# Performance work log

Hardware: AMD Instinct MI355X
Metric: run time of the kernel (lower is better)

Reference implementation:

```python
import jax, jax.numpy as jnp
import numpy as np
from jax import lax

HEADS = 8
DIM_HEAD = 64
SCALE = DIM_HEAD ** -0.5

def conv2d(x, w, stride=1, pad=0):
    return lax.conv_general_dilated(
        x, w, window_strides=(stride, stride),
        padding=[(pad, pad), (pad, pad)],
        dimension_numbers=("NCHW", "OIHW", "NCHW"))

def setup_inputs() -> dict:
    key = jax.random.key(0)
    ks = jax.random.split(key, 5)
    b, dim, H, W = 8, 256, 32, 32
    inner = HEADS * DIM_HEAD  # 512
    x = jax.random.normal(ks[0], (b, dim, H, W), jnp.float32)
    Wq = jax.random.normal(ks[1], (inner, dim, 1, 1), jnp.float32) * 0.05
    Wkv = jax.random.normal(ks[2], (2 * inner, dim, 3, 3), jnp.float32) * 0.05
    Wout = jax.random.normal(ks[3], (dim, inner, 1, 1), jnp.float32) * 0.05
    bout = jnp.zeros((dim,), jnp.float32)
    return {"x": x, "Wq": Wq, "Wkv": Wkv, "Wout": Wout, "bout": bout}

def reference(x, Wq, Wkv, Wout, bout):
    b = x.shape[0]
    h, d = HEADS, DIM_HEAD
    q = conv2d(x, Wq, stride=1, pad=0)        # [b, h*d, H, W]
    kv = conv2d(x, Wkv, stride=1, pad=1)      # [b, 2*h*d, H, W]
    k, v = jnp.split(kv, 2, axis=1)
    out_h, out_w = q.shape[-2:]

    def to_bhnd(t):
        # b (h d) x y -> b h (x y) d
        B, _, X, Y = t.shape
        return t.reshape(B, h, d, X * Y).transpose(0, 1, 3, 2)

    q, k, v = map(to_bhnd, (q, k, v))
    dots = jnp.einsum("bhid,bhjd->bhij", q, k) * SCALE
    attn = jax.nn.softmax(dots, axis=-1)
    out = jnp.einsum("bhij,bhjd->bhid", attn, v)  # [b, h, n, d]
    # b h (x y) d -> b (h d) x y
    out = out.transpose(0, 1, 3, 2).reshape(b, h * d, out_h, out_w)
    out = jax.nn.gelu(out, approximate=False)
    out = conv2d(out, Wout, stride=1, pad=0) + bout[None, :, None, None]
    return out
```

## Files before the change

### kernel.cpp

```cpp
#include <hip/hip_runtime.h>
#include <math.h>

#define BATCH 8
#define DIM   256
#define NPIX  1024
#define DHEAD 64
#define INNER 512
#define KVCH  1024
#define PPIX  1156

typedef _Float16 half8 __attribute__((ext_vector_type(8)));
typedef _Float16 half4 __attribute__((ext_vector_type(4)));
typedef float    f32x4 __attribute__((ext_vector_type(4)));
typedef float    f32x16 __attribute__((ext_vector_type(16)));
#define MFMA16(a, b, c) __builtin_amdgcn_mfma_f32_16x16x32_f16(a, b, c, 0, 0, 0)
#define MFMA32(a, b, c) __builtin_amdgcn_mfma_f32_32x32x16_f16(a, b, c, 0, 0, 0)

static __device__ __forceinline__ float gelu_f(float v) {
    return 0.5f * v * (1.0f + erff(v * 0.70710678118654752440f));
}

static __device__ __forceinline__ void gload16(const _Float16* g, _Float16* l) {
    __builtin_amdgcn_global_load_lds(
        (const __attribute__((address_space(1))) unsigned int*)g,
        (__attribute__((address_space(3))) unsigned int*)l, 16, 0, 0);
}

__global__ __launch_bounds__(256) void prep_kernel(
    const float* __restrict__ Wq, const float* __restrict__ Wkv,
    const float* __restrict__ Wout, const float* __restrict__ x,
    _Float16* __restrict__ Aq, _Float16* __restrict__ Akv,
    _Float16* __restrict__ Aout, _Float16* __restrict__ xtp)
{
    const int bid = blockIdx.x, tid = threadIdx.x;
    if (bid < 512) {
        __shared__ float ts[64][65];
        const int pt = (bid & 15) * 64, ic0 = ((bid >> 4) & 3) * 64, b = bid >> 6;
        const float* xb = x + (((size_t)(b * DIM + ic0)) << 10) + pt;
#pragma unroll
        for (int e = tid; e < 4096; e += 256) {
            int i = e >> 6, p = e & 63;
            ts[i][p] = xb[((size_t)i << 10) + p];
        }
        __syncthreads();
#pragma unroll
        for (int e = tid; e < 512; e += 256) {
            int p = e >> 3, ig = e & 7;
            int gp = pt + p, y = gp >> 5, xc = gp & 31;
            half8 v;
#pragma unroll
            for (int u = 0; u < 8; ++u) v[u] = (_Float16)ts[ig * 8 + u][p];
            *(half8*)&xtp[((size_t)b * PPIX + (y + 1) * 34 + xc + 1) * 256 + ic0 + ig * 8] = v;
        }
    } else if (bid < 10752) {
        const int e = (bid - 512) * 256 + tid;
        if (e < 131072) Aq[e] = (_Float16)Wq[e];
        const int e2 = e - 131072;
        if (e2 >= 0 && e2 < 2359296) {
            int oc = e2 / 2304, r = e2 - oc * 2304;
            int s = r >> 8, ic = r & 255;
            Akv[e2] = (_Float16)Wkv[oc * 2304 + ic * 9 + s];
        }
        const int e3 = e - 131072 - 2359296;
        if (e3 >= 0 && e3 < 131072) Aout[e3] = (_Float16)Wout[e3];
    } else {
        const int he = (bid - 10752) * 256 + tid;
        if (he < 270336) {
            int b = he / 33792;
            int r = he - b * 33792;
            int hp = r >> 8, ic = r & 255;
            int row, col;
            if (hp < 34)      { row = 0;  col = hp; }
            else if (hp < 68) { row = 33; col = hp - 34; }
            else { int k2 = hp - 68; row = 1 + (k2 >> 1); col = (k2 & 1) * 33; }
            xtp[((size_t)b * PPIX + row * 34 + col) * 256 + ic] = (_Float16)0.f;
        }
    }
}

__global__ __launch_bounds__(256) void qkv_gemm_kernel(
    const _Float16* __restrict__ Akv, const _Float16* __restrict__ Aq,
    const _Float16* __restrict__ xtp, _Float16* __restrict__ qt,
    _Float16* __restrict__ ktp, _Float16* __restrict__ vb)
{
    __shared__ _Float16 As0[128 * 64];
    __shared__ _Float16 As1[128 * 64];
    __shared__ _Float16 Bs0[128 * 64];
    __shared__ _Float16 Bs1[128 * 64];
    const int nt = blockIdx.x, mt = blockIdx.y, b = blockIdx.z;
    const bool QBLK = (mt >= 8);
    const int tid = threadIdx.x;
    const int w = tid >> 6, lane = tid & 63;
    const int l31 = lane & 31, kh = lane >> 5;
    const int m0 = (QBLK ? mt - 8 : mt) * 128, p0 = nt * 128;
    const int wm = (w >> 1) * 64, wn = (w & 1) * 64;

    const int srow = lane >> 3;
    const int scol = ((lane & 7) ^ srow) * 8;

    const _Float16* abase = QBLK ? Aq : Akv;
    const int astride = QBLK ? 256 : 2304;
    const int ktend = QBLK ? 4 : 36;

    const _Float16* agp[4];
    const _Float16* bgp[4];
#pragma unroll
    for (int c = 0; c < 4; ++c) {
        int row = (w * 4 + c) * 8 + srow;
        agp[c] = abase + (size_t)(m0 + row) * astride + scol;
        int p = p0 + row, py = p >> 5, px = p & 31;
        bgp[c] = xtp + ((size_t)b * PPIX + (py + 1) * 34 + px + 1) * 256 + scol;
    }

    f32x16 acc[2][2];
#pragma unroll
    for (int mf = 0; mf < 2; ++mf)
#pragma unroll
        for (int nf = 0; nf < 2; ++nf)
#pragma unroll
            for (int r = 0; r < 16; ++r) acc[mf][nf][r] = 0.f;

    auto STAGE = [&](int kt, _Float16* Asb, _Float16* Bsb) {
        const int s = QBLK ? 4 : (kt >> 2);
        const int doff = (s / 3 - 1) * 34 + (s - (s / 3) * 3) - 1;
        const int boff = doff * 256 + (kt & 3) * 64;
#pragma unroll
        for (int c = 0; c < 4; ++c)
            gload16(agp[c] + kt * 64, &Asb[(w * 4 + c) * 512]);
#pragma unroll
        for (int c = 0; c < 4; ++c)
            gload16(bgp[c] + boff, &Bsb[(w * 4 + c) * 512]);
    };

    auto COMPUTE = [&](const _Float16* Asb, const _Float16* Bsb) {
#pragma unroll
        for (int kc = 0; kc < 4; ++kc) {
            const int cx = ((((kc << 1) | kh) ^ (l31 & 7)) << 3);
            half8 af[2], bf[2];
#pragma unroll
            for (int mf = 0; mf < 2; ++mf)
                af[mf] = *(const half8*)&Asb[(wm + mf * 32 + l31) * 64 + cx];
#pragma unroll
            for (int nf = 0; nf < 2; ++nf)
                bf[nf] = *(const half8*)&Bsb[(wn + nf * 32 + l31) * 64 + cx];
#pragma unroll
            for (int mf = 0; mf < 2; ++mf)
#pragma unroll
                for (int nf = 0; nf < 2; ++nf)
                    acc[mf][nf] = MFMA32(af[mf], bf[nf], acc[mf][nf]);
        }
    };

    STAGE(0, As0, Bs0);
    __syncthreads();

    for (int kt2 = 0; kt2 < ktend; kt2 += 2) {
        STAGE(kt2 + 1, As1, Bs1);
        COMPUTE(As0, Bs0);
        __syncthreads();
        if (kt2 + 2 < ktend) STAGE(kt2 + 2, As0, Bs0);
        COMPUTE(As1, Bs1);
        __syncthreads();
    }

#pragma unroll
    for (int mf = 0; mf < 2; ++mf) {
        const int mbase = m0 + wm + mf * 32;
        if (!QBLK && mbase >= 512) {
#pragma unroll
            for (int nf = 0; nf < 2; ++nf) {
                const int pix = p0 + wn + nf * 32 + l31;
#pragma unroll
                for (int reg = 0; reg < 16; ++reg) {
                    const int mv = mbase - 512 + (reg & 3) + 8 * (reg >> 2) + 4 * kh;
                    vb[(((size_t)(b * 512 + mv)) << 10) + pix] =
                        (_Float16)acc[mf][nf][reg];
                }
            }
        } else {
            const int h = mbase >> 6;
            const int dbase = (mbase & 63) + kh * 4;
            _Float16* dst = QBLK ? qt : ktp;
#pragma unroll
            for (int nf = 0; nf < 2; ++nf) {
                const int pix = p0 + wn + nf * 32 + l31;
#pragma unroll
                for (int g = 0; g < 4; ++g) {
                    half4 v4;
#pragma unroll
                    for (int r = 0; r < 4; ++r) {
                        float vv = acc[mf][nf][g * 4 + r];
                        if (QBLK) vv *= 0.125f;
                        v4[r] = (_Float16)vv;
                    }
                    *(half4*)&dst[((((size_t)(b * 8 + h)) << 10) + pix) * 64 + dbase + g * 8] = v4;
                }
            }
        }
    }
}

template<int M, int K, int KROW>
__global__ __launch_bounds__(256) void out_gemm_kernel(
    const _Float16* __restrict__ A, const _Float16* __restrict__ act,
    float* __restrict__ Cout, const float* __restrict__ bias)
{
    __shared__ _Float16 As[128 * 64];
    __shared__ _Float16 Bs[64 * 64];
    const int nt = blockIdx.x, mt = blockIdx.y, b = blockIdx.z;
    const int tid = threadIdx.x;
    const int w = tid >> 6, lane = tid & 63;
    const int quad = lane >> 4, l15 = lane & 15;
    const int m0 = mt * 128, p0 = nt * 64;
    const int wm = w * 32;
    const f32x4 Z4 = {0.f, 0.f, 0.f, 0.f};

    const int srow = lane >> 3;
    const int scol = ((lane & 7) ^ srow) * 8;

    const _Float16* agp[4];
#pragma unroll
    for (int c = 0; c < 4; ++c) {
        int row = (w * 4 + c) * 8 + srow;
        agp[c] = A + (size_t)(m0 + row) * K + scol;
    }
    const _Float16* bgp[2];
#pragma unroll
    for (int c = 0; c < 2; ++c) {
        int row = (w * 2 + c) * 8 + srow;
        bgp[c] = act + (size_t)(b * NPIX + p0 + row) * KROW + scol;
    }

    f32x4 acc[2][4];
#pragma unroll
    for (int mi = 0; mi < 2; ++mi)
#pragma unroll
        for (int ni = 0; ni < 4; ++ni) acc[mi][ni] = Z4;

    for (int kt = 0; kt < K / 64; ++kt) {
        __syncthreads();
#pragma unroll
        for (int c = 0; c < 4; ++c)
            gload16(agp[c] + kt * 64, &As[(w * 4 + c) * 512]);
#pragma unroll
        for (int c = 0; c < 2; ++c)
            gload16(bgp[c] + kt * 64, &Bs[(w * 2 + c) * 512]);
        __syncthreads();
#pragma unroll
        for (int ks = 0; ks < 2; ++ks) {
            half8 av[2], bv[4];
#pragma unroll
            for (int mi = 0; mi < 2; ++mi) {
                const int r = wm + mi * 16 + l15;
                av[mi] = *(const half8*)&As[r * 64 + (((ks * 4 + quad) ^ (l15 & 7)) << 3)];
            }
#pragma unroll
            for (int ni = 0; ni < 4; ++ni) {
                const int r = ni * 16 + l15;
                bv[ni] = *(const half8*)&Bs[r * 64 + (((ks * 4 + quad) ^ (l15 & 7)) << 3)];
            }
#pragma unroll
            for (int mi = 0; mi < 2; ++mi)
#pragma unroll
                for (int ni = 0; ni < 4; ++ni)
                    acc[mi][ni] = MFMA16(av[mi], bv[ni], acc[mi][ni]);
        }
    }

#pragma unroll
    for (int mi = 0; mi < 2; ++mi) {
#pragma unroll
        for (int r = 0; r < 4; ++r) {
            const int m = m0 + wm + mi * 16 + quad * 4 + r;
            const float bv = bias[m];
#pragma unroll
            for (int ni = 0; ni < 4; ++ni) {
                const int pix = p0 + ni * 16 + l15;
                Cout[(((size_t)(b * M + m)) << 10) + pix] = acc[mi][ni][r] + bv;
            }
        }
    }
}

__global__ __launch_bounds__(256) void attn_kernel(
    const _Float16* __restrict__ qt,
    const _Float16* __restrict__ ktp,
    const _Float16* __restrict__ vbb,
    _Float16* __restrict__ gout)
{
    __shared__ _Float16 Ks[128 * 64];
    __shared__ _Float16 Vs[64 * 128];
    __shared__ _Float16 Pb[128 * 128];
    const int qtile = blockIdx.x, bh = blockIdx.y;
    const int b = bh >> 3, h = bh & 7;
    const int p0 = qtile * 128;
    const int tid = threadIdx.x;
    const int w = tid >> 6, lane = tid & 63;
    const int quad = lane >> 4, l15 = lane & 15;
    const f32x4 Z4 = {0.f, 0.f, 0.f, 0.f};

    half8 ones;
#pragma unroll
    for (int u = 0; u < 8; ++u) ones[u] = (_Float16)1.0f;

    half8 qf[2][2];
    {
        const _Float16* qrow =
            qt + ((((size_t)(bh)) << 10) + p0 + w * 32 + l15) * 64;
#pragma unroll
        for (int iff = 0; iff < 2; ++iff)
#pragma unroll
            for (int ks = 0; ks < 2; ++ks)
                qf[iff][ks] = *(const half8*)(qrow + iff * 16 * 64 + ks * 32 + quad * 8);
    }

    const _Float16* kbase = ktp + ((size_t)bh << 16);
    const _Float16* vbase = vbb + (((size_t)(b * 512 + h * 64)) << 10);

    f32x4 oacc[4][2];
#pragma unroll
    for (int mf = 0; mf < 4; ++mf)
#pragma unroll
        for (int iff = 0; iff < 2; ++iff) oacc[mf][iff] = Z4;
    f32x4 racc[2] = {Z4, Z4};

    const int kchunk = (lane & 7) ^ (lane >> 3);
    for (int kt = 0; kt < 8; ++kt) {
        const int pk = kt * 128;
        __syncthreads();
        const _Float16* kg = kbase + (size_t)pk * 64;
#pragma unroll
        for (int i = 0; i < 4; ++i) {
            const int t = i * 4 + w;
            gload16(kg + (t * 8 + (lane >> 3)) * 64 + kchunk * 8, &Ks[t * 512]);
        }
#pragma unroll
        for (int i = 0; i < 4; ++i) {
            const int t = i * 4 + w;
            const int vd = t * 4 + (lane >> 4);
            gload16(vbase + ((size_t)vd << 10) + pk + (((lane & 15) ^ (vd & 15)) << 3),
                    &Vs[t * 512]);
        }
        __syncthreads();

#pragma unroll
        for (int g = 0; g < 2; ++g) {
            f32x4 s[4][2];
#pragma unroll
            for (int jf2 = 0; jf2 < 4; ++jf2) {
                const int jr = (g * 4 + jf2) * 16 + l15;
                const half8 ka0 = *(const half8*)&Ks[jr * 64 + ((quad ^ (l15 & 7)) << 3)];
                const half8 ka1 = *(const half8*)&Ks[jr * 64 + (((4 + quad) ^ (l15 & 7)) << 3)];
#pragma unroll
                for (int iff = 0; iff < 2; ++iff) {
                    s[jf2][iff] = MFMA16(ka0, qf[iff][0], Z4);
                    s[jf2][iff] = MFMA16(ka1, qf[iff][1], s[jf2][iff]);
                }
            }
#pragma unroll
            for (int jf2 = 0; jf2 < 4; ++jf2) {
#pragma unroll
                for (int iff = 0; iff < 2; ++iff) {
                    half4 pv4;
#pragma unroll
                    for (int r = 0; r < 4; ++r)
                        pv4[r] = (_Float16)__expf(s[jf2][iff][r] - 8.0f);
                    const int i = w * 32 + iff * 16 + l15;
                    const int c = ((g * 4 + jf2) << 1) + (quad >> 1);
                    *(half4*)&Pb[i * 128 + ((c ^ l15) << 3) + ((quad & 1) << 2)] = pv4;
                }
            }
        }
#pragma unroll
        for (int kc = 0; kc < 4; ++kc) {
            half8 bv[2];
#pragma unroll
            for (int iff = 0; iff < 2; ++iff) {
                const int i = w * 32 + iff * 16 + l15;
                bv[iff] = *(const half8*)&Pb[i * 128 + (((kc * 4 + quad) ^ l15) << 3)];
                racc[iff] = MFMA16(ones, bv[iff], racc[iff]);
            }
#pragma unroll
            for (int mf = 0; mf < 4; ++mf) {
                const int vr = mf * 16 + l15;
                const half8 va = *(const half8*)&Vs[vr * 128 + (((kc * 4 + quad) ^ l15) << 3)];
#pragma unroll
                for (int iff = 0; iff < 2; ++iff)
                    oacc[mf][iff] = MFMA16(va, bv[iff], oacc[mf][iff]);
            }
        }
    }

    float rinv[2];
#pragma unroll
    for (int iff = 0; iff < 2; ++iff) rinv[iff] = 1.f / racc[iff][0];

    __syncthreads();
    _Float16* scr = Pb;
#pragma unroll
    for (int mf = 0; mf < 4; ++mf) {
#pragma unroll
        for (int iff = 0; iff < 2; ++iff) {
            half4 o4;
#pragma unroll
            for (int r = 0; r < 4; ++r)
                o4[r] = (_Float16)gelu_f(oacc[mf][iff][r] * rinv[iff]);
            const int i = w * 32 + iff * 16 + l15;
            *(half4*)&scr[i * 72 + mf * 16 + quad * 4] = o4;
        }
    }
    __syncthreads();
    _Float16* go = gout + ((size_t)(b * NPIX + p0)) * INNER + h * 64;
#pragma unroll
    for (int it = 0; it < 4; ++it) {
        const int e = tid + it * 256;
        const int p = e >> 3, dg = e & 7;
        *(half8*)(go + (size_t)p * INNER + dg * 8) = *(const half8*)&scr[p * 72 + dg * 8];
    }
}

extern "C" void kernel_launch(void* const* d_in, const int* in_sizes, int n_in,
                              void* d_out, int out_size, void* d_ws, size_t ws_size,
                              hipStream_t stream)
{
    const float* x    = (const float*)d_in[0];
    const float* Wq   = (const float*)d_in[1];
    const float* Wkv  = (const float*)d_in[2];
    const float* Wout = (const float*)d_in[3];
    const float* bout = (const float*)d_in[4];
    float* out = (float*)d_out;

    _Float16* xtp  = (_Float16*)d_ws;
    _Float16* Aq   = xtp  + (size_t)BATCH * PPIX * DIM;
    _Float16* Akv  = Aq   + (size_t)INNER * DIM;
    _Float16* Aout = Akv  + (size_t)KVCH * 2304;
    _Float16* qt   = Aout + (size_t)DIM * INNER;
    _Float16* vb   = qt   + (size_t)BATCH * NPIX * INNER;
    _Float16* ktp  = vb   + (size_t)BATCH * NPIX * INNER;
    _Float16* gout = ktp  + (size_t)BATCH * NPIX * INNER;

    prep_kernel<<<11808, 256, 0, stream>>>(Wq, Wkv, Wout, x, Aq, Akv, Aout, xtp);
    qkv_gemm_kernel<<<dim3(8, 12, BATCH), 256, 0, stream>>>(Akv, Aq, xtp, qt, ktp, vb);
    attn_kernel<<<dim3(8, 64), 256, 0, stream>>>(qt, ktp, vb, gout);
    out_gemm_kernel<DIM, 512, 512>
        <<<dim3(16, 2, BATCH), 256, 0, stream>>>(Aout, gout, out, bout);
}
```

Before: 175.4 us.

## Double-buffer LDS tiles in output GEMM and attention kernels

The output projection GEMM now ping-pongs between two LDS buffers for A and B tiles, issuing async global-to-LDS loads for the next K tile before computing on the current one. The attention kernel double-buffers K tiles and interleaves the K and V loads with the QK^T and PV phases, so memory traffic overlaps MFMA work. This targets the load-then-wait stalls of the single-buffered loops. The cost is extra LDS per block (attention grows from 64KB to 80KB), which may reduce occupancy, plus a more intricate barrier schedule.

```diff
diff --git a/kernel.cpp b/kernel.cpp
--- a/kernel.cpp
+++ b/kernel.cpp
@@ -205,8 +205,10 @@
     const _Float16* __restrict__ A, const _Float16* __restrict__ act,
     float* __restrict__ Cout, const float* __restrict__ bias)
 {
-    __shared__ _Float16 As[128 * 64];
-    __shared__ _Float16 Bs[64 * 64];
+    __shared__ _Float16 As0[128 * 64];
+    __shared__ _Float16 As1[128 * 64];
+    __shared__ _Float16 Bs0[64 * 64];
+    __shared__ _Float16 Bs1[64 * 64];
     const int nt = blockIdx.x, mt = blockIdx.y, b = blockIdx.z;
     const int tid = threadIdx.x;
     const int w = tid >> 6, lane = tid & 63;
@@ -237,27 +239,28 @@
 #pragma unroll
         for (int ni = 0; ni < 4; ++ni) acc[mi][ni] = Z4;
 
-    for (int kt = 0; kt < K / 64; ++kt) {
-        __syncthreads();
+    auto STAGE = [&](int kt, _Float16* Asb, _Float16* Bsb) {
 #pragma unroll
         for (int c = 0; c < 4; ++c)
-            gload16(agp[c] + kt * 64, &As[(w * 4 + c) * 512]);
+            gload16(agp[c] + kt * 64, &Asb[(w * 4 + c) * 512]);
 #pragma unroll
         for (int c = 0; c < 2; ++c)
-            gload16(bgp[c] + kt * 64, &Bs[(w * 2 + c) * 512]);
-        __syncthreads();
+            gload16(bgp[c] + kt * 64, &Bsb[(w * 2 + c) * 512]);
+    };
+
+    auto COMPUTE = [&](const _Float16* Asb, const _Float16* Bsb) {
 #pragma unroll
         for (int ks = 0; ks < 2; ++ks) {
             half8 av[2], bv[4];
 #pragma unroll
             for (int mi = 0; mi < 2; ++mi) {
                 const int r = wm + mi * 16 + l15;
-                av[mi] = *(const half8*)&As[r * 64 + (((ks * 4 + quad) ^ (l15 & 7)) << 3)];
+                av[mi] = *(const half8*)&Asb[r * 64 + (((ks * 4 + quad) ^ (l15 & 7)) << 3)];
             }
 #pragma unroll
             for (int ni = 0; ni < 4; ++ni) {
                 const int r = ni * 16 + l15;
-                bv[ni] = *(const half8*)&Bs[r * 64 + (((ks * 4 + quad) ^ (l15 & 7)) << 3)];
+                bv[ni] = *(const half8*)&Bsb[r * 64 + (((ks * 4 + quad) ^ (l15 & 7)) << 3)];
             }
 #pragma unroll
             for (int mi = 0; mi < 2; ++mi)
@@ -265,6 +268,17 @@
                 for (int ni = 0; ni < 4; ++ni)
                     acc[mi][ni] = MFMA16(av[mi], bv[ni], acc[mi][ni]);
         }
+    };
+
+    STAGE(0, As0, Bs0);
+    __syncthreads();
+    for (int kt2 = 0; kt2 < K / 64; kt2 += 2) {
+        STAGE(kt2 + 1, As1, Bs1);
+        COMPUTE(As0, Bs0);
+        __syncthreads();
+        if (kt2 + 2 < K / 64) STAGE(kt2 + 2, As0, Bs0);
+        COMPUTE(As1, Bs1);
+        __syncthreads();
     }
 
 #pragma unroll
@@ -288,7 +302,8 @@
     const _Float16* __restrict__ vbb,
     _Float16* __restrict__ gout)
 {
-    __shared__ _Float16 Ks[128 * 64];
+    __shared__ _Float16 Ks0[128 * 64];
+    __shared__ _Float16 Ks1[128 * 64];
     __shared__ _Float16 Vs[64 * 128];
     __shared__ _Float16 Pb[128 * 128];
     const int qtile = blockIdx.x, bh = blockIdx.y;
@@ -325,15 +340,17 @@
     f32x4 racc[2] = {Z4, Z4};
 
     const int kchunk = (lane & 7) ^ (lane >> 3);
-    for (int kt = 0; kt < 8; ++kt) {
-        const int pk = kt * 128;
-        __syncthreads();
-        const _Float16* kg = kbase + (size_t)pk * 64;
+
+    auto STAGE_K = [&](int kt, _Float16* Kb) {
+        const _Float16* kg = kbase + (size_t)(kt * 128) * 64;
 #pragma unroll
         for (int i = 0; i < 4; ++i) {
             const int t = i * 4 + w;
-            gload16(kg + (t * 8 + (lane >> 3)) * 64 + kchunk * 8, &Ks[t * 512]);
-        }
+            gload16(kg + (t * 8 + (lane >> 3)) * 64 + kchunk * 8, &Kb[t * 512]);
+        }
+    };
+    auto STAGE_V = [&](int kt) {
+        const int pk = kt * 128;
 #pragma unroll
         for (int i = 0; i < 4; ++i) {
             const int t = i * 4 + w;
@@ -341,16 +358,16 @@
             gload16(vbase + ((size_t)vd << 10) + pk + (((lane & 15) ^ (vd & 15)) << 3),
                     &Vs[t * 512]);
         }
-        __syncthreads();
-
+    };
+    auto QKT = [&](const _Float16* Kb) {
 #pragma unroll
         for (int g = 0; g < 2; ++g) {
             f32x4 s[4][2];
 #pragma unroll
             for (int jf2 = 0; jf2 < 4; ++jf2) {
                 const int jr = (g * 4 + jf2) * 16 + l15;
-                const half8 ka0 = *(const half8*)&Ks[jr * 64 + ((quad ^ (l15 & 7)) << 3)];
-                const half8 ka1 = *(const half8*)&Ks[jr * 64 + (((4 + quad) ^ (l15 & 7)) << 3)];
+                const half8 ka0 = *(const half8*)&Kb[jr * 64 + ((quad ^ (l15 & 7)) << 3)];
+                const half8 ka1 = *(const half8*)&Kb[jr * 64 + (((4 + quad) ^ (l15 & 7)) << 3)];
 #pragma unroll
                 for (int iff = 0; iff < 2; ++iff) {
                     s[jf2][iff] = MFMA16(ka0, qf[iff][0], Z4);
@@ -371,6 +388,8 @@
                 }
             }
         }
+    };
+    auto PV = [&]() {
 #pragma unroll
         for (int kc = 0; kc < 4; ++kc) {
             half8 bv[2];
@@ -389,6 +408,25 @@
                     oacc[mf][iff] = MFMA16(va, bv[iff], oacc[mf][iff]);
             }
         }
+    };
+
+    STAGE_K(0, Ks0);
+    STAGE_V(0);
+    __syncthreads();
+
+    for (int kt2 = 0; kt2 < 8; kt2 += 2) {
+        QKT(Ks0);
+        __syncthreads();
+        STAGE_K(kt2 + 1, Ks1);
+        PV();
+        __syncthreads();
+        STAGE_V(kt2 + 1);
+        QKT(Ks1);
+        __syncthreads();
+        if (kt2 + 2 < 8) STAGE_K(kt2 + 2, Ks0);
+        PV();
+        __syncthreads();
+        if (kt2 + 2 < 8) STAGE_V(kt2 + 2);
     }
 
     float rinv[2];
```

After: 177.7 us. About the same (+1.3%).
